# Optimization experiments

Measured on AMD Instinct MI355X. Metric: run time of the kernel, lower is better.

The kernel has to match this reference:

```python
import jax, jax.numpy as jnp
import numpy as np

NUM_HEADS = 16
WINDOW = 16  # hard-coded in module; half-window = 8


def sliding_mask(seq_len):
    # mask[i, j] = 0 if j in [i - W//2, i + W//2], else -inf  (additive)
    i = jnp.arange(seq_len)[:, None]
    j = jnp.arange(seq_len)[None, :]
    return jnp.where(jnp.abs(i - j) <= WINDOW // 2, 0.0, -jnp.inf).astype(jnp.float32)


def setup_inputs() -> dict:
    key = jax.random.key(0)
    k1, k2, k3 = jax.random.split(key, 3)
    B, S, D = 2, 2048, 1024
    scale = 1.0 / np.sqrt(D)
    return {
        "input_embeddings": jax.random.normal(k1, (B, S, D), dtype=jnp.float32),
        "token_ids": jax.random.randint(k2, (B, S), 0, 32000, dtype=jnp.int64),
        # nn.MultiheadAttention params: packed in_proj [3D, D] + bias, out_proj [D, D] + bias
        "w_qkv": jax.random.normal(jax.random.fold_in(k3, 0), (3 * D, D), dtype=jnp.float32) * scale,
        "b_qkv": jnp.zeros((3 * D,), dtype=jnp.float32),
        "w_out": jax.random.normal(jax.random.fold_in(k3, 1), (D, D), dtype=jnp.float32) * scale,
        "b_out": jnp.zeros((D,), dtype=jnp.float32),
    }


def reference(input_embeddings, token_ids, w_qkv, b_qkv, w_out, b_out):
    B, S, D = input_embeddings.shape
    H = NUM_HEADS
    hd = D // H
    # packed QKV projection (torch in_proj): [B, S, 3D]
    qkv = input_embeddings @ w_qkv.T + b_qkv
    q, k, v = jnp.split(qkv, 3, axis=-1)
    # [B, H, S, hd]
    q = q.reshape(B, S, H, hd).transpose(0, 2, 1, 3)
    k = k.reshape(B, S, H, hd).transpose(0, 2, 1, 3)
    v = v.reshape(B, S, H, hd).transpose(0, 2, 1, 3)
    scores = jnp.einsum("bhqd,bhkd->bhqk", q, k) / jnp.sqrt(jnp.asarray(hd, q.dtype))
    scores = scores + sliding_mask(S)  # broadcast additive [S, S] mask
    attn = jax.nn.softmax(scores, axis=-1)
    ctx = jnp.einsum("bhqk,bhkd->bhqd", attn, v)
    ctx = ctx.transpose(0, 2, 1, 3).reshape(B, S, D)
    return ctx @ w_out.T + b_out
```

## Files before the change

### kernel.cpp

```cpp
#include <hip/hip_runtime.h>
#include <stdint.h>


typedef __bf16 bf16_t;
typedef bf16_t bf16x8 __attribute__((ext_vector_type(8)));
typedef unsigned short u16x8 __attribute__((ext_vector_type(8)));
typedef float f32x4 __attribute__((ext_vector_type(4)));

#define GLD16(g, l)                                                        \
  __builtin_amdgcn_global_load_lds(                                        \
      (const __attribute__((address_space(1))) void*)(g),                  \
      (__attribute__((address_space(3))) void*)(l), 16, 0, 0)

__device__ __forceinline__ unsigned short f2bf(float f) {
  unsigned int u = __float_as_uint(f);
  u += 0x7FFFu + ((u >> 16) & 1u);
  return (unsigned short)(u >> 16);
}

__device__ __forceinline__ bf16x8 ld16(const unsigned short* p) {
  return __builtin_bit_cast(bf16x8, *reinterpret_cast<const u16x8*>(p));
}

__global__ void cvt_f32_bf16(const float* __restrict__ in,
                             unsigned short* __restrict__ out, int n4) {
  int i = blockIdx.x * blockDim.x + threadIdx.x;
  if (i >= n4) return;
  const float4 f = reinterpret_cast<const float4*>(in)[i];
  ushort4 o;
  o.x = f2bf(f.x); o.y = f2bf(f.y); o.z = f2bf(f.z); o.w = f2bf(f.w);
  reinterpret_cast<ushort4*>(out)[i] = o;
}

template <int EPI>
__global__ __launch_bounds__(256, 2) void gemm_bt(
    const unsigned short* __restrict__ A,
    const unsigned short* __restrict__ Bt,
    const float* __restrict__ bias,
    unsigned short* __restrict__ Cq, unsigned short* __restrict__ Ck,
    unsigned short* __restrict__ Cv, float* __restrict__ Cp, int M, int N,
    int K) {
  __shared__ unsigned short sA[128 * 32];
  __shared__ unsigned short sB[128 * 32];

  const int tid = threadIdx.x;
  const int wave = tid >> 6;
  const int lane = tid & 63;
  const int m0 = blockIdx.x * 128;
  const int n0 = blockIdx.y * 128;
  const int wr = wave >> 1;
  const int wc = wave & 1;

  f32x4 acc[4][4] = {};

  const int srow = tid >> 2;
  const int scol = (tid & 3) << 3;
  const unsigned short* Ag0 = A + (size_t)(m0 + srow) * K + scol;
  const unsigned short* Ag1 = Ag0 + (size_t)64 * K;
  const unsigned short* Bg0 = Bt + (size_t)(n0 + srow) * K + scol;
  const unsigned short* Bg1 = Bg0 + (size_t)64 * K;
  unsigned short* sA0 = &sA[wave * 512];
  unsigned short* sA1 = &sA[2048 + wave * 512];
  unsigned short* sB0 = &sB[wave * 512];
  unsigned short* sB1 = &sB[2048 + wave * 512];

  const int ar = wr * 64 + (lane & 15);
  const int br = wc * 64 + (lane & 15);
  const int kc = (lane >> 4) << 3;

  for (int k0 = 0; k0 < K; k0 += 32) {
    __syncthreads();
    GLD16(Ag0 + k0, sA0);
    GLD16(Ag1 + k0, sA1);
    GLD16(Bg0 + k0, sB0);
    GLD16(Bg1 + k0, sB1);
    __syncthreads();

    bf16x8 af[4], bfr[4];
#pragma unroll
    for (int f = 0; f < 4; ++f) {
      af[f] = ld16(&sA[(ar + f * 16) * 32 + kc]);
      bfr[f] = ld16(&sB[(br + f * 16) * 32 + kc]);
    }
#pragma unroll
    for (int i = 0; i < 4; ++i)
#pragma unroll
      for (int j = 0; j < 4; ++j)
        acc[i][j] =
            __builtin_amdgcn_mfma_f32_16x16x32_bf16(af[i], bfr[j], acc[i][j], 0, 0, 0);
  }

#pragma unroll
  for (int i = 0; i < 4; ++i) {
    const int row0 = m0 + wr * 64 + i * 16 + ((lane >> 4) << 2);
#pragma unroll
    for (int j = 0; j < 4; ++j) {
      const int col = n0 + wc * 64 + j * 16 + (lane & 15);
      const float bb = bias[col];
#pragma unroll
      for (int r = 0; r < 4; ++r) {
        const int m = row0 + r;
        const float val = acc[i][j][r] + bb;
        if (EPI == 0) {
          Cp[(size_t)m * N + col] = val;
        } else {
          const int b = m >> 11, s = m & 2047;
          const int which = col >> 10, nn = col & 1023;
          const int h = nn >> 6, d = nn & 63;
          const int bh = (b << 4) + h;
          const unsigned short vb = f2bf(val);
          if (which == 0)
            Cq[((size_t)(bh * 2048 + s)) * 64 + d] = vb;
          else if (which == 1)
            Ck[((size_t)(bh * 2048 + s)) * 64 + d] = vb;
          else
            Cv[((size_t)(bh * 64 + d)) * 2048 + s] = vb;
        }
      }
    }
  }
}

__global__ __launch_bounds__(256) void attn_mfma(
    const unsigned short* __restrict__ Qb, const unsigned short* __restrict__ Kb,
    const unsigned short* __restrict__ Vt, unsigned short* __restrict__ ctx) {
  __shared__ unsigned short P[4][16][40];
  const int wave = threadIdx.x >> 6;
  const int lane = threadIdx.x & 63;
  const int gw = (blockIdx.x << 2) + wave;
  const int bh = gw >> 7;
  const int i0 = (gw & 127) << 4;
  const int qr = lane & 15;
  const int kg = lane >> 4;
  const int kc = kg << 3;

  const size_t qbase = ((size_t)(bh * 2048 + i0 + qr)) * 64;
  const bf16x8 aq0 = ld16(Qb + qbase + kc);
  const bf16x8 aq1 = ld16(Qb + qbase + 32 + kc);

  f32x4 sc0 = {0.f, 0.f, 0.f, 0.f}, sc1 = {0.f, 0.f, 0.f, 0.f};
  {
    const int ka0 = i0 - 8 + qr;
    const int ka1 = ka0 + 16;
    const int kcl0 = min(max(ka0, 0), 2047);
    const int kcl1 = min(max(ka1, 0), 2047);
    const unsigned short* K0 = Kb + ((size_t)(bh * 2048 + kcl0)) * 64;
    const unsigned short* K1 = Kb + ((size_t)(bh * 2048 + kcl1)) * 64;
    sc0 = __builtin_amdgcn_mfma_f32_16x16x32_bf16(aq0, ld16(K0 + kc), sc0, 0, 0, 0);
    sc0 = __builtin_amdgcn_mfma_f32_16x16x32_bf16(aq1, ld16(K0 + 32 + kc), sc0, 0, 0, 0);
    sc1 = __builtin_amdgcn_mfma_f32_16x16x32_bf16(aq0, ld16(K1 + kc), sc1, 0, 0, 0);
    sc1 = __builtin_amdgcn_mfma_f32_16x16x32_bf16(aq1, ld16(K1 + 32 + kc), sc1, 0, 0, 0);
  }

  unsigned short* Pw = &P[wave][0][0];
  float lsum[4];
#pragma unroll
  for (int r = 0; r < 4; ++r) {
    const int q = (kg << 2) + r;
    const int key0 = qr, key1 = 16 + qr;
    const int ka0 = i0 - 8 + key0, ka1 = i0 - 8 + key1;
    const bool v0 = (q <= key0) && (key0 <= q + 16) && (ka0 >= 0) && (ka0 < 2048);
    const bool v1 = (q <= key1) && (key1 <= q + 16) && (ka1 >= 0) && (ka1 < 2048);
    const float e0 = v0 ? __expf(sc0[r] * 0.125f) : 0.f;
    const float e1 = v1 ? __expf(sc1[r] * 0.125f) : 0.f;
    Pw[q * 40 + key0] = f2bf(e0);
    Pw[q * 40 + key1] = f2bf(e1);
    float s = e0 + e1;
#pragma unroll
    for (int off = 1; off < 16; off <<= 1) s += __shfl_xor(s, off);
    lsum[r] = s;
  }

  const bf16x8 pa = ld16(&Pw[qr * 40 + kc]);

  const int base_s = min(max(i0 - 8 + kc, 0), 2040);
  f32x4 o[4];
  const f32x4 zero = {0.f, 0.f, 0.f, 0.f};
#pragma unroll
  for (int t2 = 0; t2 < 4; ++t2) {
    const unsigned short* Vr =
        Vt + ((size_t)(bh * 64 + t2 * 16 + qr)) * 2048 + base_s;
    o[t2] = __builtin_amdgcn_mfma_f32_16x16x32_bf16(pa, ld16(Vr), zero, 0, 0, 0);
  }

  const int b = bh >> 4, h = bh & 15;
  float rinv[4];
#pragma unroll
  for (int r = 0; r < 4; ++r) rinv[r] = 1.0f / lsum[r];
#pragma unroll
  for (int t2 = 0; t2 < 4; ++t2) {
#pragma unroll
    for (int r = 0; r < 4; ++r) {
      const int q = (kg << 2) + r;
      const int d = t2 * 16 + qr;
      ctx[((size_t)(b * 2048 + i0 + q)) * 1024 + (h << 6) + d] =
          f2bf(o[t2][r] * rinv[r]);
    }
  }
}

extern "C" void kernel_launch(void* const* d_in, const int* in_sizes, int n_in,
                              void* d_out, int out_size, void* d_ws,
                              size_t ws_size, hipStream_t stream) {
  const float* x = (const float*)d_in[0];
  const float* w_qkv = (const float*)d_in[2];
  const float* b_qkv = (const float*)d_in[3];
  const float* w_out = (const float*)d_in[4];
  const float* b_out = (const float*)d_in[5];
  float* out = (float*)d_out;

  char* ws = (char*)d_ws;
  unsigned short* xb    = (unsigned short*)(ws + 0);
  unsigned short* wqkvb = (unsigned short*)(ws + 8388608);
  unsigned short* woutb = (unsigned short*)(ws + 14680064);
  unsigned short* Qb    = (unsigned short*)(ws + 16777216);
  unsigned short* Kb    = (unsigned short*)(ws + 25165824);
  unsigned short* Vt    = (unsigned short*)(ws + 33554432);
  unsigned short* ctxb  = (unsigned short*)(ws + 41943040);

  cvt_f32_bf16<<<(1048576 + 255) / 256, 256, 0, stream>>>(x, xb, 1048576);
  cvt_f32_bf16<<<(786432 + 255) / 256, 256, 0, stream>>>(w_qkv, wqkvb, 786432);
  cvt_f32_bf16<<<(262144 + 255) / 256, 256, 0, stream>>>(w_out, woutb, 262144);

  gemm_bt<1><<<dim3(32, 24), 256, 0, stream>>>(xb, wqkvb, b_qkv, Qb, Kb, Vt,
                                               nullptr, 4096, 3072, 1024);

  attn_mfma<<<1024, 256, 0, stream>>>(Qb, Kb, Vt, ctxb);

  gemm_bt<0><<<dim3(32, 8), 256, 0, stream>>>(ctxb, woutb, b_out, nullptr,
                                              nullptr, nullptr, out, 4096,
                                              1024, 1024);
}
```

Measured before the change: 89.93 us.

## Double-buffer GEMM LDS tiles and use fragment-major LDS layout

The bf16 GEMM now has two LDS buffers for the A and B tiles. It prefetches the next K-slice with global_load_lds while the MFMAs run on the current slice, which leaves one barrier per iteration instead of two. The global-to-LDS mapping is also changed so each wave stores a 16-row by 32-k fragment in the exact order lanes later read it, so fragment reads become contiguous 16-byte loads and avoid bank conflicts. This doubles LDS use to 32 KB per block, which could limit occupancy, and it relies on the barrier waiting for the asynchronous LDS loads to finish.

```diff
diff --git a/kernel.cpp b/kernel.cpp
--- a/kernel.cpp
+++ b/kernel.cpp
@@ -40,8 +40,8 @@
     unsigned short* __restrict__ Cq, unsigned short* __restrict__ Ck,
     unsigned short* __restrict__ Cv, float* __restrict__ Cp, int M, int N,
     int K) {
-  __shared__ unsigned short sA[128 * 32];
-  __shared__ unsigned short sB[128 * 32];
+  __shared__ unsigned short sA[2][4096];
+  __shared__ unsigned short sB[2][4096];
 
   const int tid = threadIdx.x;
   const int wave = tid >> 6;
@@ -53,34 +53,35 @@
 
   f32x4 acc[4][4] = {};
 
-  const int srow = tid >> 2;
-  const int scol = (tid & 3) << 3;
-  const unsigned short* Ag0 = A + (size_t)(m0 + srow) * K + scol;
+  const int srow = (wave << 4) + (lane & 15);
+  const int skc = (lane >> 4) << 3;
+  const unsigned short* Ag0 = A + (size_t)(m0 + srow) * K + skc;
   const unsigned short* Ag1 = Ag0 + (size_t)64 * K;
-  const unsigned short* Bg0 = Bt + (size_t)(n0 + srow) * K + scol;
+  const unsigned short* Bg0 = Bt + (size_t)(n0 + srow) * K + skc;
   const unsigned short* Bg1 = Bg0 + (size_t)64 * K;
-  unsigned short* sA0 = &sA[wave * 512];
-  unsigned short* sA1 = &sA[2048 + wave * 512];
-  unsigned short* sB0 = &sB[wave * 512];
-  unsigned short* sB1 = &sB[2048 + wave * 512];
-
-  const int ar = wr * 64 + (lane & 15);
-  const int br = wc * 64 + (lane & 15);
-  const int kc = (lane >> 4) << 3;
-
+  const int wb0 = wave * 512;
+  const int wb1 = 2048 + wave * 512;
+
+  GLD16(Ag0, &sA[0][wb0]);
+  GLD16(Ag1, &sA[0][wb1]);
+  GLD16(Bg0, &sB[0][wb0]);
+  GLD16(Bg1, &sB[0][wb1]);
+  __syncthreads();
+
+  int cur = 0;
   for (int k0 = 0; k0 < K; k0 += 32) {
-    __syncthreads();
-    GLD16(Ag0 + k0, sA0);
-    GLD16(Ag1 + k0, sA1);
-    GLD16(Bg0 + k0, sB0);
-    GLD16(Bg1 + k0, sB1);
-    __syncthreads();
-
+    const int nxt = cur ^ 1;
+    if (k0 + 32 < K) {
+      GLD16(Ag0 + k0 + 32, &sA[nxt][wb0]);
+      GLD16(Ag1 + k0 + 32, &sA[nxt][wb1]);
+      GLD16(Bg0 + k0 + 32, &sB[nxt][wb0]);
+      GLD16(Bg1 + k0 + 32, &sB[nxt][wb1]);
+    }
     bf16x8 af[4], bfr[4];
 #pragma unroll
     for (int f = 0; f < 4; ++f) {
-      af[f] = ld16(&sA[(ar + f * 16) * 32 + kc]);
-      bfr[f] = ld16(&sB[(br + f * 16) * 32 + kc]);
+      af[f] = ld16(&sA[cur][(wr * 256 + f * 64 + lane) * 8]);
+      bfr[f] = ld16(&sB[cur][(wc * 256 + f * 64 + lane) * 8]);
     }
 #pragma unroll
     for (int i = 0; i < 4; ++i)
@@ -88,6 +89,8 @@
       for (int j = 0; j < 4; ++j)
         acc[i][j] =
             __builtin_amdgcn_mfma_f32_16x16x32_bf16(af[i], bfr[j], acc[i][j], 0, 0, 0);
+    __syncthreads();
+    cur = nxt;
   }
 
 #pragma unroll
```

Result: slower. 114.8 us (+27.6%).

## Double GEMM K-tile to 64 with XOR-swizzled LDS and merge conversion kernels

Applied to the files above, without the earlier changes.

The GEMM now stages 64-wide K slices per iteration instead of 32, which halves the number of barrier pairs. It stores the slices in LDS with an XOR swizzle on the 16-byte slot index to avoid bank conflicts on the fragment reads. The three fp32-to-bf16 conversion launches are merged into one grid-stride kernel to cut launch overhead. LDS use doubles to 32KB per block, which may limit occupancy.

```diff
diff --git a/kernel.cpp b/kernel.cpp
--- a/kernel.cpp
+++ b/kernel.cpp
@@ -22,14 +22,24 @@
   return __builtin_bit_cast(bf16x8, *reinterpret_cast<const u16x8*>(p));
 }
 
-__global__ void cvt_f32_bf16(const float* __restrict__ in,
-                             unsigned short* __restrict__ out, int n4) {
-  int i = blockIdx.x * blockDim.x + threadIdx.x;
-  if (i >= n4) return;
-  const float4 f = reinterpret_cast<const float4*>(in)[i];
-  ushort4 o;
-  o.x = f2bf(f.x); o.y = f2bf(f.y); o.z = f2bf(f.z); o.w = f2bf(f.w);
-  reinterpret_cast<ushort4*>(out)[i] = o;
+__global__ void cvt_all(const float* __restrict__ x, const float* __restrict__ wq,
+                        const float* __restrict__ wo, unsigned short* __restrict__ xb,
+                        unsigned short* __restrict__ wqb,
+                        unsigned short* __restrict__ wob) {
+  const int N0 = 1048576, N1 = 786432, N2 = 262144;
+  for (int i = blockIdx.x * blockDim.x + threadIdx.x; i < N0 + N1 + N2;
+       i += gridDim.x * blockDim.x) {
+    const float4* src;
+    unsigned short* dst;
+    int j;
+    if (i < N0) { src = (const float4*)x; dst = xb; j = i; }
+    else if (i < N0 + N1) { src = (const float4*)wq; dst = wqb; j = i - N0; }
+    else { src = (const float4*)wo; dst = wob; j = i - N0 - N1; }
+    const float4 f = src[j];
+    ushort4 o;
+    o.x = f2bf(f.x); o.y = f2bf(f.y); o.z = f2bf(f.z); o.w = f2bf(f.w);
+    reinterpret_cast<ushort4*>(dst)[j] = o;
+  }
 }
 
 template <int EPI>
@@ -40,8 +50,8 @@
     unsigned short* __restrict__ Cq, unsigned short* __restrict__ Ck,
     unsigned short* __restrict__ Cv, float* __restrict__ Cp, int M, int N,
     int K) {
-  __shared__ unsigned short sA[128 * 32];
-  __shared__ unsigned short sB[128 * 32];
+  __shared__ unsigned short sA[128 * 64];
+  __shared__ unsigned short sB[128 * 64];
 
   const int tid = threadIdx.x;
   const int wave = tid >> 6;
@@ -53,41 +63,44 @@
 
   f32x4 acc[4][4] = {};
 
-  const int srow = tid >> 2;
-  const int scol = (tid & 3) << 3;
-  const unsigned short* Ag0 = A + (size_t)(m0 + srow) * K + scol;
-  const unsigned short* Ag1 = Ag0 + (size_t)64 * K;
-  const unsigned short* Bg0 = Bt + (size_t)(n0 + srow) * K + scol;
-  const unsigned short* Bg1 = Bg0 + (size_t)64 * K;
-  unsigned short* sA0 = &sA[wave * 512];
-  unsigned short* sA1 = &sA[2048 + wave * 512];
-  unsigned short* sB0 = &sB[wave * 512];
-  unsigned short* sB1 = &sB[2048 + wave * 512];
-
-  const int ar = wr * 64 + (lane & 15);
-  const int br = wc * 64 + (lane & 15);
-  const int kc = (lane >> 4) << 3;
-
-  for (int k0 = 0; k0 < K; k0 += 32) {
+  const int srow = (wave << 3) + (lane >> 3);
+  const int sslot = ((lane & 7) ^ (lane >> 3)) << 3;
+  const unsigned short* Ag = A + (size_t)(m0 + srow) * K + sslot;
+  const unsigned short* Bg = Bt + (size_t)(n0 + srow) * K + sslot;
+  const int wdst = wave * 512;
+
+  const int kg = lane >> 4;
+  const int l7 = lane & 7;
+
+  for (int k0 = 0; k0 < K; k0 += 64) {
     __syncthreads();
-    GLD16(Ag0 + k0, sA0);
-    GLD16(Ag1 + k0, sA1);
-    GLD16(Bg0 + k0, sB0);
-    GLD16(Bg1 + k0, sB1);
+#pragma unroll
+    for (int r = 0; r < 4; ++r) {
+      GLD16(Ag + (size_t)(r * 32) * K + k0, &sA[r * 2048 + wdst]);
+      GLD16(Bg + (size_t)(r * 32) * K + k0, &sB[r * 2048 + wdst]);
+    }
     __syncthreads();
 
-    bf16x8 af[4], bfr[4];
-#pragma unroll
-    for (int f = 0; f < 4; ++f) {
-      af[f] = ld16(&sA[(ar + f * 16) * 32 + kc]);
-      bfr[f] = ld16(&sB[(br + f * 16) * 32 + kc]);
-    }
-#pragma unroll
-    for (int i = 0; i < 4; ++i)
-#pragma unroll
-      for (int j = 0; j < 4; ++j)
-        acc[i][j] =
-            __builtin_amdgcn_mfma_f32_16x16x32_bf16(af[i], bfr[j], acc[i][j], 0, 0, 0);
+    bf16x8 af[2][4], bfr[2][4];
+#pragma unroll
+    for (int st = 0; st < 2; ++st) {
+#pragma unroll
+      for (int f = 0; f < 4; ++f) {
+        const int ar = wr * 64 + f * 16 + (lane & 15);
+        const int br = wc * 64 + f * 16 + (lane & 15);
+        const int se = ((st << 2) | kg) ^ l7;
+        af[st][f] = ld16(&sA[ar * 64 + (se << 3)]);
+        bfr[st][f] = ld16(&sB[br * 64 + (se << 3)]);
+      }
+    }
+#pragma unroll
+    for (int st = 0; st < 2; ++st)
+#pragma unroll
+      for (int i = 0; i < 4; ++i)
+#pragma unroll
+        for (int j = 0; j < 4; ++j)
+          acc[i][j] = __builtin_amdgcn_mfma_f32_16x16x32_bf16(
+              af[st][i], bfr[st][j], acc[i][j], 0, 0, 0);
   }
 
 #pragma unroll
@@ -218,9 +231,7 @@
   unsigned short* Vt    = (unsigned short*)(ws + 33554432);
   unsigned short* ctxb  = (unsigned short*)(ws + 41943040);
 
-  cvt_f32_bf16<<<(1048576 + 255) / 256, 256, 0, stream>>>(x, xb, 1048576);
-  cvt_f32_bf16<<<(786432 + 255) / 256, 256, 0, stream>>>(w_qkv, wqkvb, 786432);
-  cvt_f32_bf16<<<(262144 + 255) / 256, 256, 0, stream>>>(w_out, woutb, 262144);
+  cvt_all<<<2048, 256, 0, stream>>>(x, w_qkv, w_out, xb, wqkvb, woutb);
 
   gemm_bt<1><<<dim3(32, 24), 256, 0, stream>>>(xb, wqkvb, b_qkv, Qb, Kb, Vt,
                                                nullptr, 4096, 3072, 1024);
```

After: 80.40 us. -10.6%, faster.
